# Kernel tuning notes

Hardware: AMD Instinct MI355X
Metric: run time of the kernel (lower is better)

## Reference

```python
import jax, jax.numpy as jnp
import numpy as np

B, S, D_IN, E, H = 2, 2048, 1024, 1024, 16  # batch, seq, input_size, embedding_size, heads


def setup_inputs() -> dict:
    key = jax.random.key(0)
    k1, k2, k3 = jax.random.split(key, 3)
    x = jax.random.normal(k1, (B, S, D_IN), dtype=jnp.float32)
    # fused QKV projection weight stored as [in, 3E] (torch Linear weight transposed)
    W0 = jax.random.normal(k2, (D_IN, 3 * E), dtype=jnp.float32) * (1.0 / np.sqrt(D_IN))
    b0 = jax.random.normal(k3, (3 * E,), dtype=jnp.float32) * 0.02
    return {"x": x, "W0": W0, "b0": b0}


def reference(x, W0, b0):
    b, s, _ = x.shape
    y = x @ W0 + b0                              # [B,S,3E]
    y = y.reshape(b, s, H, -1).transpose(0, 2, 1, 3)  # [B,H,S,3*head_dim]
    q, k, v = jnp.split(y, 3, axis=-1)           # each [B,H,S,head_dim]
    scale = 1.0 / jnp.sqrt(jnp.asarray(D_IN, dtype=x.dtype))  # NB: sqrt(input_size), as in source
    scores = jnp.einsum("bhqd,bhkd->bhqk", q, k) * scale
    # causal mask: -inf above diagonal
    causal = jnp.triu(jnp.full((s, s), -jnp.inf, dtype=scores.dtype), k=1)
    scores = scores + causal
    attn = jax.nn.softmax(scores, axis=-1)       # [B,H,S,S]
    o = jnp.einsum("bhqk,bhkd->bhqd", attn, v)   # [B,H,S,head_dim]
    # faithful to source: reshape directly from (B,H,S,d) to (B,S,H*d) WITHOUT permuting back
    return o.reshape(b, s, -1)
```

## Files before the change

kernel.cpp:

```cpp
#include <hip/hip_runtime.h>
#include <stdint.h>

typedef __attribute__((ext_vector_type(4))) float f32x4;
typedef __attribute__((ext_vector_type(16))) float f32x16;
typedef __attribute__((ext_vector_type(8))) short bf16x8;
typedef __attribute__((ext_vector_type(4))) short bf16x4;

#define MFMA16(a, b, c) __builtin_amdgcn_mfma_f32_16x16x32_bf16((a), (b), (c), 0, 0, 0)
#define MFMA32(a, b, c) __builtin_amdgcn_mfma_f32_32x32x16_bf16((a), (b), (c), 0, 0, 0)

__device__ __forceinline__ short f2bf(float f) {
    union { float f; uint32_t u; } v; v.f = f;
    uint32_t r = (v.u + 0x7fffu + ((v.u >> 16) & 1u)) >> 16;
    return (short)(uint16_t)r;
}
__device__ __forceinline__ float bf2f(short s) {
    union { uint32_t u; float f; } v; v.u = ((uint32_t)(uint16_t)s) << 16;
    return v.f;
}

__device__ __forceinline__ void async_ld16(const short* g, short* l) {
    __builtin_amdgcn_global_load_lds(
        (const __attribute__((address_space(1))) uint32_t*)g,
        (__attribute__((address_space(3))) uint32_t*)l, 16, 0, 0);
}

#define MK_BFRAG(C, O, OUT) do {                                                   \
    uint32_t a_, b_, c_, d_;                                                       \
    asm("v_cvt_pk_bf16_f32 %0, %1, %2" : "=v"(a_) : "v"((C)[(O)+0]), "v"((C)[(O)+1])); \
    asm("v_cvt_pk_bf16_f32 %0, %1, %2" : "=v"(c_) : "v"((C)[(O)+2]), "v"((C)[(O)+3])); \
    asm("v_cvt_pk_bf16_f32 %0, %1, %2" : "=v"(b_) : "v"((C)[(O)+4]), "v"((C)[(O)+5])); \
    asm("v_cvt_pk_bf16_f32 %0, %1, %2" : "=v"(d_) : "v"((C)[(O)+6]), "v"((C)[(O)+7])); \
    asm("v_permlane32_swap_b32 %0, %1" : "+v"(a_), "+v"(b_));                      \
    asm("v_permlane32_swap_b32 %0, %1" : "+v"(c_), "+v"(d_));                      \
    union { uint32_t u[4]; bf16x8 v; } pb_;                                        \
    pb_.u[0] = a_; pb_.u[1] = c_; pb_.u[2] = b_; pb_.u[3] = d_;                    \
    OUT = pb_.v;                                                                   \
} while (0)

__global__ __launch_bounds__(256)
void convert_x(const float* __restrict__ X, short* __restrict__ Xb) {
    const int i8 = (blockIdx.x * 256 + threadIdx.x) << 3;
    f32x4 a = *(const f32x4*)(X + i8);
    f32x4 b = *(const f32x4*)(X + i8 + 4);
    bf16x8 o;
#pragma unroll
    for (int j = 0; j < 4; ++j) { o[j] = f2bf(a[j]); o[4 + j] = f2bf(b[j]); }
    *(bf16x8*)(Xb + i8) = o;
}

__global__ __launch_bounds__(256)
void convert_wt(const float* __restrict__ W, short* __restrict__ Wt) {
    __shared__ short T[64][72];
    const int t = threadIdx.x;
    const int n0 = blockIdx.x * 64, k0 = blockIdx.y * 64;
#pragma unroll
    for (int i = 0; i < 4; ++i) {
        const int r = i * 16 + (t >> 4);
        const int c = (t & 15) << 2;
        f32x4 v = *(const f32x4*)(W + (size_t)(k0 + r) * 3072 + n0 + c);
#pragma unroll
        for (int j = 0; j < 4; ++j) T[c + j][r] = f2bf(v[j]);
    }
    __syncthreads();
#pragma unroll
    for (int i = 0; i < 2; ++i) {
        const int r = i * 32 + (t >> 3);
        const int c = (t & 7) << 3;
        *(bf16x8*)(Wt + (size_t)(n0 + r) * 1024 + k0 + c) = *(const bf16x8*)&T[r][c];
    }
}

__global__ __launch_bounds__(256, 2)
void gemm_pack(const short* __restrict__ Xb, const short* __restrict__ Wt,
               const float* __restrict__ bias, short* __restrict__ Qp,
               short* __restrict__ Kp, short* __restrict__ Vp) {
    __shared__ short Asm[2][128 * 32];
    __shared__ short Bsm[2][128 * 32];

    const int tid  = threadIdx.x;
    const int lane = tid & 63;
    const int l15  = lane & 15;
    const int lq   = lane >> 4;
    const int wave = tid >> 6;
    const int wr = wave >> 1, wc = wave & 1;

    const int bid = blockIdx.x;
    const int swz = (bid & 7) * 96 + (bid >> 3);
    const int m0 = (swz / 24) * 128, n0 = (swz % 24) * 128;

    const int srow = tid >> 2;
    const int scol = (tid & 3) << 3;

    f32x4 acc[4][4];
#pragma unroll
    for (int m = 0; m < 4; ++m)
#pragma unroll
        for (int n = 0; n < 4; ++n) acc[m][n] = (f32x4)(0.0f);

    auto stage = [&](int k0, int bb) {
#pragma unroll
        for (int i = 0; i < 2; ++i)
            async_ld16(Xb + (size_t)(m0 + i * 64 + srow) * 1024 + k0 + scol,
                       &Asm[bb][(i * 256 + wave * 64) * 8]);
#pragma unroll
        for (int i = 0; i < 2; ++i)
            async_ld16(Wt + (size_t)(n0 + i * 64 + srow) * 1024 + k0 + scol,
                       &Bsm[bb][(i * 256 + wave * 64) * 8]);
    };

    auto compute = [&](int bb) {
        bf16x8 af[4], bfv[4];
#pragma unroll
        for (int m = 0; m < 4; ++m)
            af[m] = *(const bf16x8*)&Asm[bb][(wr * 64 + m * 16 + l15) * 32 + (lq << 3)];
#pragma unroll
        for (int n = 0; n < 4; ++n)
            bfv[n] = *(const bf16x8*)&Bsm[bb][(wc * 64 + n * 16 + l15) * 32 + (lq << 3)];
#pragma unroll
        for (int m = 0; m < 4; ++m)
#pragma unroll
            for (int n = 0; n < 4; ++n) acc[m][n] = MFMA16(af[m], bfv[n], acc[m][n]);
    };

    stage(0, 0);
    __syncthreads();
    int cur = 0;
#pragma unroll 1
    for (int kt = 0; kt < 32; ++kt) {
        if (kt + 1 < 32) stage((kt + 1) * 32, cur ^ 1);
        compute(cur);
        __syncthreads();
        cur ^= 1;
    }

    const float SCALE2 = 0.03125f * 1.44269504f;
    float bv[4];
#pragma unroll
    for (int n = 0; n < 4; ++n) bv[n] = bias[n0 + wc * 64 + n * 16 + l15];

    const size_t bbase = (size_t)(m0 >> 11) * 2097152;
    const int tokb = (m0 & 2047) + wr * 64;

#pragma unroll
    for (int n = 0; n < 4; ++n) {
        const int col = n0 + wc * 64 + n * 16 + l15;
        const int h   = col / 192;
        const int seg = (col >> 6) % 3;
        const int d   = col & 63;
        const size_t hb = bbase + (size_t)h * 131072;
        if (seg == 0) {
            const int cp = ((d >> 4) << 9) + (((d >> 3) & 1) << 8) + (d & 7);
#pragma unroll
            for (int m = 0; m < 4; ++m)
#pragma unroll
                for (int r = 0; r < 4; ++r) {
                    const int tok = tokb + m * 16 + (lq << 2) + r;
                    Qp[hb + ((size_t)(tok >> 5) << 11) + ((tok & 31) << 3) + cp] =
                        f2bf((acc[m][n][r] + bv[n]) * SCALE2);
                }
        } else if (seg == 1) {
            const int cp = ((d >> 4) << 10) + (((d >> 3) & 1) << 8) + (d & 7);
#pragma unroll
            for (int m = 0; m < 4; ++m)
#pragma unroll
                for (int r = 0; r < 4; ++r) {
                    const int tok = tokb + m * 16 + (lq << 2) + r;
                    Kp[hb + ((size_t)(tok >> 6) << 12) + (((tok >> 5) & 1) << 9)
                       + ((tok & 31) << 3) + cp] = f2bf(acc[m][n][r] + bv[n]);
                }
        } else {
            const int cp = ((d >> 5) << 11) + ((d & 31) << 3);
#pragma unroll
            for (int m = 0; m < 4; ++m)
#pragma unroll
                for (int r = 0; r < 4; ++r) {
                    const int tok = tokb + m * 16 + (lq << 2) + r;
                    Vp[hb + ((size_t)(tok >> 6) << 12) + (((tok >> 4) & 3) << 9)
                       + (((tok >> 3) & 1) << 8) + (tok & 7) + cp] =
                        f2bf(acc[m][n][r] + bv[n]);
                }
        }
    }
}

__global__ __launch_bounds__(64, 3)
void attn_part(const short* __restrict__ Qp, const short* __restrict__ Kp,
               const short* __restrict__ Vp, short* __restrict__ Po,
               float* __restrict__ Pm) {
    const int tid = threadIdx.x;
    const int l31 = tid & 31;
    const int hi  = tid >> 5;
    const int bh = blockIdx.y;
    const int u  = blockIdx.x;

    int qt, t0, t1;
    if (u < 32)      { qt = u + 32; t0 = 0;  t1 = 16; }
    else if (u < 64) { qt = 95 - u; t0 = 16; t1 = (qt >> 1) + 1; }
    else             { qt = u - 64; t0 = 0;  t1 = (qt >> 1) + 1; }
    const bool hasDiag = (u >= 32);
    const int q0 = qt * 32;

    const size_t hb = (size_t)bh * 131072;

    bf16x8 qf[4];
    {
        const short* qp = Qp + hb + qt * 2048 + tid * 8;
#pragma unroll
        for (int dg = 0; dg < 4; ++dg) qf[dg] = *(const bf16x8*)(qp + dg * 512);
    }
    const short* kb = Qp ? Kp + hb + (size_t)t0 * 4096 + tid * 8 : nullptr;
    const short* vb = Vp + hb + (size_t)t0 * 4096 + tid * 8;

    f32x16 o0 = (f32x16)(0.f), o1 = (f32x16)(0.f);
    float m_run = -1e30f, l_run = 0.f;
    const int qg = q0 + l31;

    auto tile_body = [&](int kv0, bool DIAG) {
        f32x16 c0 = (f32x16)(0.f), c1 = (f32x16)(0.f);
#pragma unroll
        for (int dg = 0; dg < 4; ++dg) {
            bf16x8 a0 = *(const bf16x8*)(kb + dg * 1024);
            bf16x8 a1 = *(const bf16x8*)(kb + dg * 1024 + 512);
            c0 = MFMA32(a0, qf[dg], c0);
            c1 = MFMA32(a1, qf[dg], c1);
        }
        bf16x8 va[8];
#pragma unroll
        for (int f = 0; f < 8; ++f) va[f] = *(const bf16x8*)(vb + f * 512);

        if (DIAG) {
#pragma unroll
            for (int r = 0; r < 16; ++r) {
                const int kvr = kv0 + (r & 3) + 8 * (r >> 2) + 4 * hi;
                if (kvr > qg)      c0[r] = -1e30f;
                if (kvr + 32 > qg) c1[r] = -1e30f;
            }
        }

        float mr[8];
#pragma unroll
        for (int r = 0; r < 8; ++r)
            mr[r] = fmaxf(fmaxf(c0[r], c0[8 + r]), fmaxf(c1[r], c1[8 + r]));
        float mx = fmaxf(fmaxf(fmaxf(mr[0], mr[1]), fmaxf(mr[2], mr[3])),
                         fmaxf(fmaxf(mr[4], mr[5]), fmaxf(mr[6], mr[7])));
        mx = fmaxf(mx, __shfl_xor(mx, 32, 64));

        if (!__all(mx <= m_run + 8.f)) {
            const float mnew = fmaxf(m_run, mx);
            const float corr = exp2f(m_run - mnew);
            l_run *= corr;
            o0 = o0 * corr;
            o1 = o1 * corr;
            m_run = mnew;
        }

        float ps0 = 0.f, ps1 = 0.f, ps2 = 0.f, ps3 = 0.f;
#pragma unroll
        for (int r = 0; r < 4; ++r) {
            c0[r]      = exp2f(c0[r]      - m_run); ps0 += c0[r];
            c0[4 + r]  = exp2f(c0[4 + r]  - m_run); ps1 += c0[4 + r];
            c0[8 + r]  = exp2f(c0[8 + r]  - m_run); ps2 += c0[8 + r];
            c0[12 + r] = exp2f(c0[12 + r] - m_run); ps3 += c0[12 + r];
        }
#pragma unroll
        for (int r = 0; r < 4; ++r) {
            c1[r]      = exp2f(c1[r]      - m_run); ps0 += c1[r];
            c1[4 + r]  = exp2f(c1[4 + r]  - m_run); ps1 += c1[4 + r];
            c1[8 + r]  = exp2f(c1[8 + r]  - m_run); ps2 += c1[8 + r];
            c1[12 + r] = exp2f(c1[12 + r] - m_run); ps3 += c1[12 + r];
        }
        l_run += (ps0 + ps1) + (ps2 + ps3);

        bf16x8 bf00, bf01, bf10, bf11;
        MK_BFRAG(c0, 0, bf00);
        MK_BFRAG(c0, 8, bf01);
        MK_BFRAG(c1, 0, bf10);
        MK_BFRAG(c1, 8, bf11);

        o0 = MFMA32(va[0], bf00, o0);
        o0 = MFMA32(va[1], bf01, o0);
        o0 = MFMA32(va[2], bf10, o0);
        o0 = MFMA32(va[3], bf11, o0);
        o1 = MFMA32(va[4], bf00, o1);
        o1 = MFMA32(va[5], bf01, o1);
        o1 = MFMA32(va[6], bf10, o1);
        o1 = MFMA32(va[7], bf11, o1);
    };

#pragma unroll 1
    for (int t = t0; t < t1 - 1; ++t) {
        tile_body(t * 64, false);
        kb += 4096;
        vb += 4096;
    }
    tile_body((t1 - 1) * 64, hasDiag);

    const float l_tot = l_run + __shfl_xor(l_run, 32, 64);
    const float inv = 1.f / l_tot;
    const int prow = (bh * 96 + u) * 32 + l31;
#pragma unroll
    for (int g = 0; g < 4; ++g) {
        bf16x4 w4;
#pragma unroll
        for (int j = 0; j < 4; ++j) w4[j] = f2bf(o0[g * 4 + j] * inv);
        *(bf16x4*)&Po[(size_t)prow * 64 + 8 * g + 4 * hi] = w4;
#pragma unroll
        for (int j = 0; j < 4; ++j) w4[j] = f2bf(o1[g * 4 + j] * inv);
        *(bf16x4*)&Po[(size_t)prow * 64 + 32 + 8 * g + 4 * hi] = w4;
    }
    if (hi == 0) Pm[prow] = m_run + __log2f(l_tot);
}

__global__ __launch_bounds__(256)
void attn_combine(const short* __restrict__ Po, const float* __restrict__ Pm,
                  float* __restrict__ Out) {
    const int idx = blockIdx.x * 256 + threadIdx.x;
    const int d4 = (idx & 15) << 2;
    const int rg = idx >> 4;
    const int q  = rg & 2047;
    const int bh = rg >> 11;
    const int qt32 = q >> 5, r = q & 31;

    f32x4 ov;
    if (qt32 < 32) {
        const int p0 = (bh * 96 + 64 + qt32) * 32 + r;
        bf16x4 a = *(const bf16x4*)&Po[(size_t)p0 * 64 + d4];
#pragma unroll
        for (int j = 0; j < 4; ++j) ov[j] = bf2f(a[j]);
    } else {
        const int p0 = (bh * 96 + (qt32 - 32)) * 32 + r;
        const int p1 = (bh * 96 + (95 - qt32)) * 32 + r;
        bf16x4 a = *(const bf16x4*)&Po[(size_t)p0 * 64 + d4];
        bf16x4 c = *(const bf16x4*)&Po[(size_t)p1 * 64 + d4];
        const float m0 = Pm[p0], m1 = Pm[p1];
        const float M = fmaxf(m0, m1);
        const float w0 = exp2f(m0 - M), w1 = exp2f(m1 - M);
        const float inv = 1.f / (w0 + w1);
#pragma unroll
        for (int j = 0; j < 4; ++j) ov[j] = (w0 * bf2f(a[j]) + w1 * bf2f(c[j])) * inv;
    }
    *(f32x4*)&Out[(size_t)rg * 64 + d4] = ov;
}

extern "C" void kernel_launch(void* const* d_in, const int* in_sizes, int n_in,
                              void* d_out, int out_size, void* d_ws, size_t ws_size,
                              hipStream_t stream) {
    const float* x  = (const float*)d_in[0];
    const float* W0 = (const float*)d_in[1];
    const float* b0 = (const float*)d_in[2];
    float* out = (float*)d_out;
    char* ws = (char*)d_ws;

    const size_t SEG_B = (size_t)32 * 131072 * 2;
    const size_t QKV_B = 3 * SEG_B;
    const size_t XBF_B = (size_t)4096 * 1024 * 2;
    const size_t PO_B  = (size_t)32 * 96 * 32 * 64 * 2;

    short* qp = (short*)ws;
    short* kp = (short*)(ws + SEG_B);
    short* vp = (short*)(ws + 2 * SEG_B);
    short* xb = (short*)(ws + QKV_B);
    short* wt = (short*)(ws + QKV_B + XBF_B);
    short* po = (short*)(ws + QKV_B);
    float* pm = (float*)(ws + QKV_B + PO_B);

    convert_x<<<dim3(2048), dim3(256), 0, stream>>>(x, xb);
    convert_wt<<<dim3(48, 16), dim3(256), 0, stream>>>(W0, wt);
    gemm_pack<<<dim3(768), dim3(256), 0, stream>>>(xb, wt, b0, qp, kp, vp);
    attn_part<<<dim3(96, 32), dim3(64), 0, stream>>>(qp, kp, vp, po, pm);
    attn_combine<<<dim3(4096), dim3(256), 0, stream>>>(po, pm, out);
}
```

Before: 103.8 us.

## Double-buffer K tiles in registers, remap blocks per XCD, use raw v_exp

The attention partial kernel now prefetches the next K tile into a second register buffer while the current tile's softmax and PV products run, unrolling the KV loop by two. The grid is flattened and remapped so that all blocks for a given set of heads land on the same XCD, which is meant to improve L2 reuse of K/V. exp2f is replaced with the raw v_exp_f32 instruction, and launch bounds drop to two waves per SIMD to make room for the extra registers. The cost is higher register pressure and lower occupancy.

```diff
diff --git a/kernel.cpp b/kernel.cpp
--- a/kernel.cpp
+++ b/kernel.cpp
@@ -17,6 +17,9 @@
 __device__ __forceinline__ float bf2f(short s) {
     union { uint32_t u; float f; } v; v.u = ((uint32_t)(uint16_t)s) << 16;
     return v.f;
+}
+__device__ __forceinline__ float fast_exp2(float x) {
+    float r; asm("v_exp_f32 %0, %1" : "=v"(r) : "v"(x)); return r;
 }
 
 __device__ __forceinline__ void async_ld16(const short* g, short* l) {
@@ -184,15 +187,19 @@
     }
 }
 
-__global__ __launch_bounds__(64, 3)
+__global__ __launch_bounds__(64, 2)
 void attn_part(const short* __restrict__ Qp, const short* __restrict__ Kp,
                const short* __restrict__ Vp, short* __restrict__ Po,
                float* __restrict__ Pm) {
     const int tid = threadIdx.x;
     const int l31 = tid & 31;
     const int hi  = tid >> 5;
-    const int bh = blockIdx.y;
-    const int u  = blockIdx.x;
+
+    const int id  = blockIdx.x;
+    const int xcd = id & 7;
+    const int idx = id >> 3;
+    const int bh  = xcd * 4 + idx / 96;
+    const int u   = idx % 96;
 
     int qt, t0, t1;
     if (u < 32)      { qt = u + 32; t0 = 0;  t1 = 16; }
@@ -209,26 +216,33 @@
 #pragma unroll
         for (int dg = 0; dg < 4; ++dg) qf[dg] = *(const bf16x8*)(qp + dg * 512);
     }
-    const short* kb = Qp ? Kp + hb + (size_t)t0 * 4096 + tid * 8 : nullptr;
-    const short* vb = Vp + hb + (size_t)t0 * 4096 + tid * 8;
 
     f32x16 o0 = (f32x16)(0.f), o1 = (f32x16)(0.f);
     float m_run = -1e30f, l_run = 0.f;
     const int qg = q0 + l31;
 
-    auto tile_body = [&](int kv0, bool DIAG) {
-        f32x16 c0 = (f32x16)(0.f), c1 = (f32x16)(0.f);
+    bf16x8 kA[8], kB[8], va[8];
+
+    auto loadK = [&](bf16x8 (&kr)[8], int t) {
+        const short* p = Kp + hb + (size_t)t * 4096 + tid * 8;
+#pragma unroll
+        for (int f = 0; f < 8; ++f)
+            kr[f] = *(const bf16x8*)(p + (f >> 1) * 1024 + (f & 1) * 512);
+    };
+    auto loadV = [&](int t) {
+        const short* p = Vp + hb + (size_t)t * 4096 + tid * 8;
+#pragma unroll
+        for (int f = 0; f < 8; ++f) va[f] = *(const bf16x8*)(p + f * 512);
+    };
+    auto qk = [&](bf16x8 (&kr)[8], f32x16& c0, f32x16& c1) {
 #pragma unroll
         for (int dg = 0; dg < 4; ++dg) {
-            bf16x8 a0 = *(const bf16x8*)(kb + dg * 1024);
-            bf16x8 a1 = *(const bf16x8*)(kb + dg * 1024 + 512);
-            c0 = MFMA32(a0, qf[dg], c0);
-            c1 = MFMA32(a1, qf[dg], c1);
-        }
-        bf16x8 va[8];
-#pragma unroll
-        for (int f = 0; f < 8; ++f) va[f] = *(const bf16x8*)(vb + f * 512);
-
+            c0 = MFMA32(kr[2 * dg],     qf[dg], c0);
+            c1 = MFMA32(kr[2 * dg + 1], qf[dg], c1);
+        }
+    };
+
+    auto smpv = [&](f32x16& c0, f32x16& c1, int kv0, bool DIAG) {
         if (DIAG) {
 #pragma unroll
             for (int r = 0; r < 16; ++r) {
@@ -248,7 +262,7 @@
 
         if (!__all(mx <= m_run + 8.f)) {
             const float mnew = fmaxf(m_run, mx);
-            const float corr = exp2f(m_run - mnew);
+            const float corr = fast_exp2(m_run - mnew);
             l_run *= corr;
             o0 = o0 * corr;
             o1 = o1 * corr;
@@ -258,17 +272,17 @@
         float ps0 = 0.f, ps1 = 0.f, ps2 = 0.f, ps3 = 0.f;
 #pragma unroll
         for (int r = 0; r < 4; ++r) {
-            c0[r]      = exp2f(c0[r]      - m_run); ps0 += c0[r];
-            c0[4 + r]  = exp2f(c0[4 + r]  - m_run); ps1 += c0[4 + r];
-            c0[8 + r]  = exp2f(c0[8 + r]  - m_run); ps2 += c0[8 + r];
-            c0[12 + r] = exp2f(c0[12 + r] - m_run); ps3 += c0[12 + r];
+            c0[r]      = fast_exp2(c0[r]      - m_run); ps0 += c0[r];
+            c0[4 + r]  = fast_exp2(c0[4 + r]  - m_run); ps1 += c0[4 + r];
+            c0[8 + r]  = fast_exp2(c0[8 + r]  - m_run); ps2 += c0[8 + r];
+            c0[12 + r] = fast_exp2(c0[12 + r] - m_run); ps3 += c0[12 + r];
         }
 #pragma unroll
         for (int r = 0; r < 4; ++r) {
-            c1[r]      = exp2f(c1[r]      - m_run); ps0 += c1[r];
-            c1[4 + r]  = exp2f(c1[4 + r]  - m_run); ps1 += c1[4 + r];
-            c1[8 + r]  = exp2f(c1[8 + r]  - m_run); ps2 += c1[8 + r];
-            c1[12 + r] = exp2f(c1[12 + r] - m_run); ps3 += c1[12 + r];
+            c1[r]      = fast_exp2(c1[r]      - m_run); ps0 += c1[r];
+            c1[4 + r]  = fast_exp2(c1[4 + r]  - m_run); ps1 += c1[4 + r];
+            c1[8 + r]  = fast_exp2(c1[8 + r]  - m_run); ps2 += c1[8 + r];
+            c1[12 + r] = fast_exp2(c1[12 + r] - m_run); ps3 += c1[12 + r];
         }
         l_run += (ps0 + ps1) + (ps2 + ps3);
 
@@ -288,13 +302,37 @@
         o1 = MFMA32(va[7], bf11, o1);
     };
 
+    int t = t0;
+    loadK(kA, t0);
 #pragma unroll 1
-    for (int t = t0; t < t1 - 1; ++t) {
-        tile_body(t * 64, false);
-        kb += 4096;
-        vb += 4096;
-    }
-    tile_body((t1 - 1) * 64, hasDiag);
+    for (; t + 2 < t1; t += 2) {
+        f32x16 c0 = (f32x16)(0.f), c1 = (f32x16)(0.f);
+        qk(kA, c0, c1);
+        loadK(kB, t + 1);
+        loadV(t);
+        smpv(c0, c1, t * 64, false);
+        f32x16 d0 = (f32x16)(0.f), d1 = (f32x16)(0.f);
+        qk(kB, d0, d1);
+        loadK(kA, t + 2);
+        loadV(t + 1);
+        smpv(d0, d1, (t + 1) * 64, false);
+    }
+    if (t + 1 < t1) {
+        f32x16 c0 = (f32x16)(0.f), c1 = (f32x16)(0.f);
+        qk(kA, c0, c1);
+        loadK(kB, t + 1);
+        loadV(t);
+        smpv(c0, c1, t * 64, false);
+        f32x16 d0 = (f32x16)(0.f), d1 = (f32x16)(0.f);
+        qk(kB, d0, d1);
+        loadV(t + 1);
+        smpv(d0, d1, (t + 1) * 64, hasDiag);
+    } else {
+        f32x16 c0 = (f32x16)(0.f), c1 = (f32x16)(0.f);
+        qk(kA, c0, c1);
+        loadV(t);
+        smpv(c0, c1, t * 64, hasDiag);
+    }
 
     const float l_tot = l_run + __shfl_xor(l_run, 32, 64);
     const float inv = 1.f / l_tot;
@@ -368,6 +406,6 @@
     convert_x<<<dim3(2048), dim3(256), 0, stream>>>(x, xb);
     convert_wt<<<dim3(48, 16), dim3(256), 0, stream>>>(W0, wt);
     gemm_pack<<<dim3(768), dim3(256), 0, stream>>>(xb, wt, b0, qp, kp, vp);
-    attn_part<<<dim3(96, 32), dim3(64), 0, stream>>>(qp, kp, vp, po, pm);
+    attn_part<<<dim3(3072), dim3(64), 0, stream>>>(qp, kp, vp, po, pm);
     attn_combine<<<dim3(4096), dim3(256), 0, stream>>>(po, pm, out);
 }
```

Result: faster. 94.51 us (-9.0%).
